# Performance work log

Measured on AMD Instinct MI355X. Metric: run time of the kernel, lower is better.

Reference implementation:

```python
import jax, jax.numpy as jnp
import numpy as np

B, N_STATES, STATE_SIZE = 32768, 16, 32
ENC, HID, OUT = 64, 128, 8


def setup_inputs() -> dict:
    key = jax.random.key(0)
    ks = jax.random.split(key, 8)
    states = jax.random.normal(ks[0], (B, N_STATES, STATE_SIZE), dtype=jnp.float32)
    # validity flags: first element of each per-field state. agent state (index 0)
    # always valid; neighbor states valid with prob 0.7 (contiguity enforced in reference
    # via cumprod, matching the original while-loop semantics).
    flags = (jax.random.uniform(ks[1], (B, N_STATES)) < 0.7).astype(jnp.float32)
    flags = flags.at[:, 0].set(1.0)
    states = states.at[:, :, 0].set(flags)
    obs_flat = states.reshape(B, N_STATES * STATE_SIZE)
    s = 0.05
    return {
        "obs_flat": obs_flat,
        "W_enc": jax.random.normal(ks[2], (STATE_SIZE, ENC), dtype=jnp.float32) * s,
        "b_enc": jnp.zeros((ENC,), dtype=jnp.float32),
        "W_f": jax.random.normal(ks[3], (2 * ENC, HID), dtype=jnp.float32) * s,
        "b_f": jnp.zeros((HID,), dtype=jnp.float32),
        "W_dec": jax.random.normal(ks[4], (HID, OUT), dtype=jnp.float32) * s,
        "b_dec": jnp.zeros((OUT,), dtype=jnp.float32),
    }


def reference(obs_flat, W_enc, b_enc, W_f, b_f, W_dec, b_dec):
    Bsz = obs_flat.shape[0]
    states = obs_flat.reshape(Bsz, N_STATES, STATE_SIZE)          # [B,N,S]
    flags = states[:, :, 0]                                        # [B,N]
    # original: while-loop stops at first invalid state -> contiguous-prefix validity
    neigh_valid = jnp.cumprod((flags[:, 1:] == 1.0).astype(jnp.float32), axis=1)  # [B,N-1]
    enc = jax.nn.relu(jnp.einsum('bns,se->bne', states, W_enc) + b_enc)            # [B,N,E]
    agent_enc = enc[:, 0]                                          # [B,E]
    neigh_enc = enc[:, 1:]                                         # [B,N-1,E]
    cnt = jnp.sum(neigh_valid, axis=1)                             # [B]
    # mean aggregation over valid neighbors; zero vector if none (original aggregates [zeros])
    agg = jnp.einsum('bne,bn->be', neigh_enc, neigh_valid) / jnp.maximum(cnt, 1.0)[:, None]
    f_in = jnp.concatenate([agent_enc, agg], axis=-1)              # [B,2E]
    hidden = jax.nn.relu(f_in @ W_f + b_f)                         # [B,H]
    logits = hidden @ W_dec + b_dec                                # [B,O]
    return logits
```

## Files before the change

kernel.cpp:

```cpp
#include <hip/hip_runtime.h>
#include <stdint.h>

#define NB    32768
#define NS    16
#define SS    32
#define ENCD  64
#define HIDD  128
#define OUTD  8
#define BT    16
#define THREADS 256

typedef _Float16 half8  __attribute__((ext_vector_type(8)));
typedef __fp16   fp16x2 __attribute__((ext_vector_type(2)));
typedef float    f32x4  __attribute__((ext_vector_type(4)));

#define MFMA(a, b, c) __builtin_amdgcn_mfma_f32_16x16x32_f16((a), (b), (c), 0, 0, 0)

__device__ __forceinline__ void split8(const float* f, half8& hi, half8& lo) {
#pragma unroll
  for (int j = 0; j < 8; j += 2) {
    fp16x2 h  = __builtin_amdgcn_cvt_pkrtz(f[j], f[j + 1]);
    float  r0 = f[j]     - (float)h[0];
    float  r1 = f[j + 1] - (float)h[1];
    fp16x2 l2 = __builtin_amdgcn_cvt_pkrtz(r0, r1);
    hi[j] = (_Float16)(float)h[0];  hi[j + 1] = (_Float16)(float)h[1];
    lo[j] = (_Float16)(float)l2[0]; lo[j + 1] = (_Float16)(float)l2[1];
  }
}

__global__ __launch_bounds__(THREADS, 6)
void gnn_fused(const float* __restrict__ obs,
               const float* __restrict__ W_enc,
               const float* __restrict__ b_enc,
               const float* __restrict__ W_f,
               const float* __restrict__ b_f,
               const float* __restrict__ W_dec,
               const float* __restrict__ b_dec,
               float* __restrict__ out)
{
  __shared__ __align__(16) float f_in[BT][132];
  __shared__ __align__(16) float hidn[BT][132];

  const int tid  = threadIdx.x;
  const int w    = tid >> 6;
  const int l    = tid & 63;
  const int m15  = l & 15;
  const int quad = l >> 4;
  const int b0   = blockIdx.x * BT;

  half8 we_hi[4], we_lo[4];
  float benc[4];
#pragma unroll
  for (int nt = 0; nt < 4; ++nt) {
    float f[8];
#pragma unroll
    for (int j = 0; j < 8; ++j)
      f[j] = W_enc[(size_t)(quad * 8 + j) * ENCD + nt * 16 + m15];
    split8(f, we_hi[nt], we_lo[nt]);
    benc[nt] = b_enc[nt * 16 + m15];
  }

  const float* bp = obs + (size_t)(b0 + w * 4) * (NS * SS) + m15 * SS + quad * 8;
  float4 c0 = ((const float4*)bp)[0];
  float4 c1 = ((const float4*)bp)[1];
#pragma unroll
  for (int i = 0; i < 4; ++i) {
    float4 n0, n1;
    if (i < 3) {
      const float* np = bp + (size_t)(i + 1) * (NS * SS);
      n0 = ((const float4*)np)[0];
      n1 = ((const float4*)np)[1];
    } else { n0 = c0; n1 = c1; }

    float f[8] = {c0.x, c0.y, c0.z, c0.w, c1.x, c1.y, c1.z, c1.w};

    unsigned long long bal = __ballot((l < 16) && (f[0] == 1.0f));
    int run = __builtin_ctzll(~(bal >> 1));
    float inv = 1.0f / fmaxf((float)run, 1.0f);

    half8 ahi, alo;
    split8(f, ahi, alo);

    const int bi = w * 4 + i;
#pragma unroll
    for (int nt = 0; nt < 4; ++nt) {
      f32x4 acc = {0.f, 0.f, 0.f, 0.f};
      acc = MFMA(ahi, we_hi[nt], acc);
      acc = MFMA(alo, we_hi[nt], acc);
      acc = MFMA(ahi, we_lo[nt], acc);
      float s = 0.f, e0 = 0.f;
#pragma unroll
      for (int r = 0; r < 4; ++r) {
        int n = quad * 4 + r;
        float v = fmaxf(acc[r] + benc[nt], 0.f);
        if (n == 0) e0 = v;
        if (n >= 1 && n <= run) s += v;
      }
      s += __shfl_xor(s, 16, 64);
      s += __shfl_xor(s, 32, 64);
      if (quad == 0) {
        f_in[bi][nt * 16 + m15]      = e0;
        f_in[bi][64 + nt * 16 + m15] = s * inv;
      }
    }
    c0 = n0; c1 = n1;
  }
  __syncthreads();

  {
    half8 fa_hi[4], fa_lo[4];
#pragma unroll
    for (int ks = 0; ks < 4; ++ks) {
      const float4* p = (const float4*)&f_in[m15][ks * 32 + quad * 8];
      float4 a = p[0], b = p[1];
      float f[8] = {a.x, a.y, a.z, a.w, b.x, b.y, b.z, b.w};
      split8(f, fa_hi[ks], fa_lo[ks]);
    }

#pragma unroll
    for (int tt = 0; tt < 2; ++tt) {
      const int h0 = (w * 2 + tt) * 16 + m15;
      f32x4 acc = {0.f, 0.f, 0.f, 0.f};
#pragma unroll
      for (int ks = 0; ks < 4; ++ks) {
        float f[8];
#pragma unroll
        for (int j = 0; j < 8; ++j)
          f[j] = W_f[(size_t)(ks * 32 + quad * 8 + j) * HIDD + h0];
        half8 bhi, blo;
        split8(f, bhi, blo);
        acc = MFMA(fa_hi[ks], bhi, acc);
        acc = MFMA(fa_lo[ks], bhi, acc);
        acc = MFMA(fa_hi[ks], blo, acc);
      }
      const float bfv = b_f[h0];
#pragma unroll
      for (int r = 0; r < 4; ++r)
        hidn[quad * 4 + r][h0] = fmaxf(acc[r] + bfv, 0.f);
    }
  }
  __syncthreads();

  if (w == 0) {
    half8 ga_hi[4], ga_lo[4];
#pragma unroll
    for (int ks = 0; ks < 4; ++ks) {
      const float4* p = (const float4*)&hidn[m15][ks * 32 + quad * 8];
      float4 a = p[0], b = p[1];
      float f[8] = {a.x, a.y, a.z, a.w, b.x, b.y, b.z, b.w};
      split8(f, ga_hi[ks], ga_lo[ks]);
    }
    f32x4 acc = {0.f, 0.f, 0.f, 0.f};
#pragma unroll
    for (int ks = 0; ks < 4; ++ks) {
      float f[8];
#pragma unroll
      for (int j = 0; j < 8; ++j) {
        int k = ks * 32 + quad * 8 + j;
        f[j] = (m15 < OUTD) ? W_dec[(size_t)k * OUTD + m15] : 0.f;
      }
      half8 bhi, blo;
      split8(f, bhi, blo);
      acc = MFMA(ga_hi[ks], bhi, acc);
      acc = MFMA(ga_lo[ks], bhi, acc);
      acc = MFMA(ga_hi[ks], blo, acc);
    }
    if (m15 < OUTD) {
      const float bd = b_dec[m15];
#pragma unroll
      for (int r = 0; r < 4; ++r) {
        const int m = quad * 4 + r;
        out[(size_t)(b0 + m) * OUTD + m15] = acc[r] + bd;
      }
    }
  }
}

extern "C" void kernel_launch(void* const* d_in, const int* in_sizes, int n_in,
                              void* d_out, int out_size, void* d_ws, size_t ws_size,
                              hipStream_t stream) {
  (void)in_sizes; (void)n_in; (void)d_ws; (void)ws_size; (void)out_size;
  const float* obs   = (const float*)d_in[0];
  const float* W_enc = (const float*)d_in[1];
  const float* b_enc = (const float*)d_in[2];
  const float* W_f   = (const float*)d_in[3];
  const float* b_f   = (const float*)d_in[4];
  const float* W_dec = (const float*)d_in[5];
  const float* b_dec = (const float*)d_in[6];
  float* out = (float*)d_out;

  dim3 grid(NB / BT);
  dim3 block(THREADS);
  gnn_fused<<<grid, block, 0, stream>>>(obs, W_enc, b_enc, W_f, b_f, W_dec, b_dec, out);
}
```

Baseline: 112.3 us.

## Pre-split weights into fp16 hi/lo in workspace and batch input loads

Adds a small prologue kernel that converts W_enc, W_f and W_dec into transposed fp16 hi/lo pairs in the workspace each call. The main kernel then loads these with vector half8 loads instead of doing strided scalar fp32 loads and per-block splitting. It also issues all four input-row loads up front rather than double-buffering them, and lowers the occupancy hint from 6 to 5. The cost is an extra kernel launch and higher register pressure from holding all the prefetched rows.

```diff
diff --git a/kernel.cpp b/kernel.cpp
--- a/kernel.cpp
+++ b/kernel.cpp
@@ -10,6 +10,14 @@
 #define BT    16
 #define THREADS 256
 
+#define WENC_HI 0
+#define WENC_LO 2048
+#define WF_HI   4096
+#define WF_LO   20480
+#define WDEC_HI 36864
+#define WDEC_LO 38912
+#define WS_HALVES 40960
+
 typedef _Float16 half8  __attribute__((ext_vector_type(8)));
 typedef __fp16   fp16x2 __attribute__((ext_vector_type(2)));
 typedef float    f32x4  __attribute__((ext_vector_type(4)));
@@ -28,13 +36,38 @@
   }
 }
 
-__global__ __launch_bounds__(THREADS, 6)
+__global__ __launch_bounds__(256)
+void presplit_w(const float* __restrict__ W_enc,
+                const float* __restrict__ W_f,
+                const float* __restrict__ W_dec,
+                _Float16* __restrict__ ws)
+{
+  const int idx = blockIdx.x * 256 + threadIdx.x;
+  float v; int hi_off, lo_off;
+  if (idx < 2048) {
+    const int e = idx >> 5, k = idx & 31;
+    v = W_enc[k * ENCD + e];
+    hi_off = WENC_HI + idx; lo_off = WENC_LO + idx;
+  } else if (idx < 2048 + 16384) {
+    const int j = idx - 2048, h = j >> 7, k = j & 127;
+    v = W_f[k * HIDD + h];
+    hi_off = WF_HI + j; lo_off = WF_LO + j;
+  } else {
+    const int j = idx - 18432, o = j >> 7, k = j & 127;
+    v = (o < OUTD) ? W_dec[k * OUTD + o] : 0.f;
+    hi_off = WDEC_HI + j; lo_off = WDEC_LO + j;
+  }
+  const _Float16 h = (_Float16)v;
+  const _Float16 l = (_Float16)(v - (float)h);
+  ws[hi_off] = h;
+  ws[lo_off] = l;
+}
+
+__global__ __launch_bounds__(THREADS, 5)
 void gnn_fused(const float* __restrict__ obs,
-               const float* __restrict__ W_enc,
+               const _Float16* __restrict__ wsp,
                const float* __restrict__ b_enc,
-               const float* __restrict__ W_f,
                const float* __restrict__ b_f,
-               const float* __restrict__ W_dec,
                const float* __restrict__ b_dec,
                float* __restrict__ out)
 {
@@ -48,31 +81,29 @@
   const int quad = l >> 4;
   const int b0   = blockIdx.x * BT;
 
+  const float* bp = obs + (size_t)(b0 + w * 4) * (NS * SS) + m15 * SS + quad * 8;
+  float4 d0[4], d1[4];
+#pragma unroll
+  for (int i = 0; i < 4; ++i) {
+    const float4* p = (const float4*)(bp + (size_t)i * (NS * SS));
+    d0[i] = p[0];
+    d1[i] = p[1];
+  }
+
   half8 we_hi[4], we_lo[4];
   float benc[4];
 #pragma unroll
   for (int nt = 0; nt < 4; ++nt) {
-    float f[8];
-#pragma unroll
-    for (int j = 0; j < 8; ++j)
-      f[j] = W_enc[(size_t)(quad * 8 + j) * ENCD + nt * 16 + m15];
-    split8(f, we_hi[nt], we_lo[nt]);
-    benc[nt] = b_enc[nt * 16 + m15];
-  }
-
-  const float* bp = obs + (size_t)(b0 + w * 4) * (NS * SS) + m15 * SS + quad * 8;
-  float4 c0 = ((const float4*)bp)[0];
-  float4 c1 = ((const float4*)bp)[1];
+    const int o = (nt * 16 + m15) * SS + quad * 8;
+    we_hi[nt] = *(const half8*)(wsp + WENC_HI + o);
+    we_lo[nt] = *(const half8*)(wsp + WENC_LO + o);
+    benc[nt]  = b_enc[nt * 16 + m15];
+  }
+
 #pragma unroll
   for (int i = 0; i < 4; ++i) {
-    float4 n0, n1;
-    if (i < 3) {
-      const float* np = bp + (size_t)(i + 1) * (NS * SS);
-      n0 = ((const float4*)np)[0];
-      n1 = ((const float4*)np)[1];
-    } else { n0 = c0; n1 = c1; }
-
-    float f[8] = {c0.x, c0.y, c0.z, c0.w, c1.x, c1.y, c1.z, c1.w};
+    float f[8] = {d0[i].x, d0[i].y, d0[i].z, d0[i].w,
+                  d1[i].x, d1[i].y, d1[i].z, d1[i].w};
 
     unsigned long long bal = __ballot((l < 16) && (f[0] == 1.0f));
     int run = __builtin_ctzll(~(bal >> 1));
@@ -103,7 +134,6 @@
         f_in[bi][64 + nt * 16 + m15] = s * inv;
       }
     }
-    c0 = n0; c1 = n1;
   }
   __syncthreads();
 
@@ -123,12 +153,9 @@
       f32x4 acc = {0.f, 0.f, 0.f, 0.f};
 #pragma unroll
       for (int ks = 0; ks < 4; ++ks) {
-        float f[8];
-#pragma unroll
-        for (int j = 0; j < 8; ++j)
-          f[j] = W_f[(size_t)(ks * 32 + quad * 8 + j) * HIDD + h0];
-        half8 bhi, blo;
-        split8(f, bhi, blo);
+        const int o = h0 * HIDD + ks * 32 + quad * 8;
+        half8 bhi = *(const half8*)(wsp + WF_HI + o);
+        half8 blo = *(const half8*)(wsp + WF_LO + o);
         acc = MFMA(fa_hi[ks], bhi, acc);
         acc = MFMA(fa_lo[ks], bhi, acc);
         acc = MFMA(fa_hi[ks], blo, acc);
@@ -153,14 +180,9 @@
     f32x4 acc = {0.f, 0.f, 0.f, 0.f};
 #pragma unroll
     for (int ks = 0; ks < 4; ++ks) {
-      float f[8];
-#pragma unroll
-      for (int j = 0; j < 8; ++j) {
-        int k = ks * 32 + quad * 8 + j;
-        f[j] = (m15 < OUTD) ? W_dec[(size_t)k * OUTD + m15] : 0.f;
-      }
-      half8 bhi, blo;
-      split8(f, bhi, blo);
+      const int o = m15 * HIDD + ks * 32 + quad * 8;
+      half8 bhi = *(const half8*)(wsp + WDEC_HI + o);
+      half8 blo = *(const half8*)(wsp + WDEC_LO + o);
       acc = MFMA(ga_hi[ks], bhi, acc);
       acc = MFMA(ga_lo[ks], bhi, acc);
       acc = MFMA(ga_hi[ks], blo, acc);
@@ -179,7 +201,7 @@
 extern "C" void kernel_launch(void* const* d_in, const int* in_sizes, int n_in,
                               void* d_out, int out_size, void* d_ws, size_t ws_size,
                               hipStream_t stream) {
-  (void)in_sizes; (void)n_in; (void)d_ws; (void)ws_size; (void)out_size;
+  (void)in_sizes; (void)n_in; (void)ws_size; (void)out_size;
   const float* obs   = (const float*)d_in[0];
   const float* W_enc = (const float*)d_in[1];
   const float* b_enc = (const float*)d_in[2];
@@ -188,8 +210,9 @@
   const float* W_dec = (const float*)d_in[5];
   const float* b_dec = (const float*)d_in[6];
   float* out = (float*)d_out;
-
-  dim3 grid(NB / BT);
-  dim3 block(THREADS);
-  gnn_fused<<<grid, block, 0, stream>>>(obs, W_enc, b_enc, W_f, b_f, W_dec, b_dec, out);
-}
+  _Float16* ws = (_Float16*)d_ws;
+
+  presplit_w<<<dim3(80), dim3(256), 0, stream>>>(W_enc, W_f, W_dec, ws);
+  gnn_fused<<<dim3(NB / BT), dim3(THREADS), 0, stream>>>(obs, ws, b_enc, b_f,
+                                                         b_dec, b_dec ? out : out);
+}
```

Result: slower. 121.3 us (+8.1%).

## Software-pipeline obs and weight loads with double buffering across stages

Applied to the files above, without the earlier changes.

Two batch rows of observations are issued up front, ahead of the W_enc load and split, and fenced with a sched_barrier so those loads go out first. The encoder loop now keeps a two-deep prefetch ring. The W_f and W_dec stages are flattened into single loops that prefetch the next weight chunk while the current chunk's MFMAs run, meant to hide global-load latency. In exchange it uses more registers, which under launch_bounds(256,6) could cause spills or lower occupancy.

```diff
diff --git a/kernel.cpp b/kernel.cpp
--- a/kernel.cpp
+++ b/kernel.cpp
@@ -48,6 +48,16 @@
   const int quad = l >> 4;
   const int b0   = blockIdx.x * BT;
 
+  const float* bp = obs + (size_t)(b0 + w * 4) * (NS * SS) + m15 * SS + quad * 8;
+  float4 A0[2], A1[2];
+  {
+    const float4* p0 = (const float4*)bp;
+    const float4* p1 = (const float4*)(bp + (size_t)(NS * SS));
+    A0[0] = p0[0]; A1[0] = p0[1];
+    A0[1] = p1[0]; A1[1] = p1[1];
+  }
+  __builtin_amdgcn_sched_barrier(0);
+
   half8 we_hi[4], we_lo[4];
   float benc[4];
 #pragma unroll
@@ -60,19 +70,15 @@
     benc[nt] = b_enc[nt * 16 + m15];
   }
 
-  const float* bp = obs + (size_t)(b0 + w * 4) * (NS * SS) + m15 * SS + quad * 8;
-  float4 c0 = ((const float4*)bp)[0];
-  float4 c1 = ((const float4*)bp)[1];
 #pragma unroll
   for (int i = 0; i < 4; ++i) {
-    float4 n0, n1;
-    if (i < 3) {
-      const float* np = bp + (size_t)(i + 1) * (NS * SS);
-      n0 = ((const float4*)np)[0];
-      n1 = ((const float4*)np)[1];
-    } else { n0 = c0; n1 = c1; }
-
-    float f[8] = {c0.x, c0.y, c0.z, c0.w, c1.x, c1.y, c1.z, c1.w};
+    const int sl = i & 1;
+    float f[8] = {A0[sl].x, A0[sl].y, A0[sl].z, A0[sl].w,
+                  A1[sl].x, A1[sl].y, A1[sl].z, A1[sl].w};
+    if (i < 2) {
+      const float4* p = (const float4*)(bp + (size_t)(i + 2) * (NS * SS));
+      A0[sl] = p[0]; A1[sl] = p[1];
+    }
 
     unsigned long long bal = __ballot((l < 16) && (f[0] == 1.0f));
     int run = __builtin_ctzll(~(bal >> 1));
@@ -103,7 +109,6 @@
         f_in[bi][64 + nt * 16 + m15] = s * inv;
       }
     }
-    c0 = n0; c1 = n1;
   }
   __syncthreads();
 
@@ -116,27 +121,40 @@
       float f[8] = {a.x, a.y, a.z, a.w, b.x, b.y, b.z, b.w};
       split8(f, fa_hi[ks], fa_lo[ks]);
     }
-
-#pragma unroll
-    for (int tt = 0; tt < 2; ++tt) {
-      const int h0 = (w * 2 + tt) * 16 + m15;
-      f32x4 acc = {0.f, 0.f, 0.f, 0.f};
-#pragma unroll
-      for (int ks = 0; ks < 4; ++ks) {
-        float f[8];
+    const float bf0 = b_f[(w * 2) * 16 + m15];
+    const float bf1 = b_f[(w * 2 + 1) * 16 + m15];
+
+    float cur[8], nxt[8];
+#pragma unroll
+    for (int j = 0; j < 8; ++j)
+      cur[j] = W_f[(size_t)(quad * 8 + j) * HIDD + (w * 2) * 16 + m15];
+
+    f32x4 acc = {0.f, 0.f, 0.f, 0.f};
+#pragma unroll
+    for (int s = 0; s < 8; ++s) {
+      const int tt = s >> 2, ks = s & 3;
+      if (s < 7) {
+        const int nt2 = (s + 1) >> 2, nk = (s + 1) & 3;
+        const int hn  = (w * 2 + nt2) * 16 + m15;
 #pragma unroll
         for (int j = 0; j < 8; ++j)
-          f[j] = W_f[(size_t)(ks * 32 + quad * 8 + j) * HIDD + h0];
-        half8 bhi, blo;
-        split8(f, bhi, blo);
-        acc = MFMA(fa_hi[ks], bhi, acc);
-        acc = MFMA(fa_lo[ks], bhi, acc);
-        acc = MFMA(fa_hi[ks], blo, acc);
-      }
-      const float bfv = b_f[h0];
-#pragma unroll
-      for (int r = 0; r < 4; ++r)
-        hidn[quad * 4 + r][h0] = fmaxf(acc[r] + bfv, 0.f);
+          nxt[j] = W_f[(size_t)(nk * 32 + quad * 8 + j) * HIDD + hn];
+      }
+      half8 bhi, blo;
+      split8(cur, bhi, blo);
+      acc = MFMA(fa_hi[ks], bhi, acc);
+      acc = MFMA(fa_lo[ks], bhi, acc);
+      acc = MFMA(fa_hi[ks], blo, acc);
+      if (ks == 3) {
+        const int   hc  = (w * 2 + tt) * 16 + m15;
+        const float bfv = tt ? bf1 : bf0;
+#pragma unroll
+        for (int r = 0; r < 4; ++r)
+          hidn[quad * 4 + r][hc] = fmaxf(acc[r] + bfv, 0.f);
+        acc = (f32x4){0.f, 0.f, 0.f, 0.f};
+      }
+#pragma unroll
+      for (int j = 0; j < 8; ++j) cur[j] = nxt[j];
     }
   }
   __syncthreads();
@@ -150,28 +168,38 @@
       float f[8] = {a.x, a.y, a.z, a.w, b.x, b.y, b.z, b.w};
       split8(f, ga_hi[ks], ga_lo[ks]);
     }
+    const float bd = (m15 < OUTD) ? b_dec[m15] : 0.f;
+
+    float cur[8], nxt[8];
+#pragma unroll
+    for (int j = 0; j < 8; ++j)
+      cur[j] = (m15 < OUTD) ? W_dec[(size_t)(quad * 8 + j) * OUTD + m15] : 0.f;
+
     f32x4 acc = {0.f, 0.f, 0.f, 0.f};
 #pragma unroll
     for (int ks = 0; ks < 4; ++ks) {
-      float f[8];
-#pragma unroll
-      for (int j = 0; j < 8; ++j) {
-        int k = ks * 32 + quad * 8 + j;
-        f[j] = (m15 < OUTD) ? W_dec[(size_t)k * OUTD + m15] : 0.f;
+      if (ks < 3) {
+#pragma unroll
+        for (int j = 0; j < 8; ++j) {
+          int k = (ks + 1) * 32 + quad * 8 + j;
+          nxt[j] = (m15 < OUTD) ? W_dec[(size_t)k * OUTD + m15] : 0.f;
+        }
       }
       half8 bhi, blo;
-      split8(f, bhi, blo);
+      split8(cur, bhi, blo);
       acc = MFMA(ga_hi[ks], bhi, acc);
       acc = MFMA(ga_lo[ks], bhi, acc);
       acc = MFMA(ga_hi[ks], blo, acc);
+      if (ks < 3) {
+#pragma unroll
+        for (int j = 0; j < 8; ++j) cur[j] = nxt[j];
+      }
     }
     if (m15 < OUTD) {
-      const float bd = b_dec[m15];
-#pragma unroll
-      for (int r = 0; r < 4; ++r) {
-        const int m = quad * 4 + r;
-        out[(size_t)(b0 + m) * OUTD + m15] = acc[r] + bd;
-      }
+      const int m0 = quad * 4;
+#pragma unroll
+      for (int r = 0; r < 4; ++r)
+        out[(size_t)(b0 + m0 + r) * OUTD + m15] = acc[r] + bd;
     }
   }
 }
```

Result: slower. 120.0 us (+6.9%).
